# Optimization experiments

Hardware: AMD Instinct MI355X
Metric: run time of the kernel (lower is better)

The kernel has to match this reference:

```python
import jax, jax.numpy as jnp
import numpy as np

N_HEADS, EMB_DIM, K_DIM, V_DIM = 16, 1024, 64, 64
B, L = 4, 2048


def setup_inputs() -> dict:
    key = jax.random.key(0)
    ks = jax.random.split(key, 7)
    scale = 1.0 / np.sqrt(EMB_DIM)
    return {
        "query": jax.random.normal(ks[0], (B, L, EMB_DIM), dtype=jnp.float32),
        "key": jax.random.normal(ks[1], (B, L, EMB_DIM), dtype=jnp.float32),
        "value": jax.random.normal(ks[2], (B, L, EMB_DIM), dtype=jnp.float32),
        "pad_mask": jnp.ones((B, L), dtype=jnp.int32),
        # Linear weights stored as (in, out); torch Linear computes x @ W.T with W (out, in)
        "Wq": jax.random.normal(ks[3], (EMB_DIM, N_HEADS * K_DIM), dtype=jnp.float32) * scale,
        "Wk": jax.random.normal(ks[4], (EMB_DIM, N_HEADS * K_DIM), dtype=jnp.float32) * scale,
        "Wv": jax.random.normal(ks[5], (EMB_DIM, N_HEADS * V_DIM), dtype=jnp.float32) * scale,
        "Wo": jax.random.normal(ks[6], (N_HEADS * V_DIM, EMB_DIM), dtype=jnp.float32) * scale,
    }


def reference(query, key, value, pad_mask, Wq, Wk, Wv, Wo):
    batch, Lq, _ = query.shape
    Lk = key.shape[1]
    # projections -> [B, L, H, dk/dv]
    q = (query @ Wq).reshape(batch, Lq, N_HEADS, K_DIM)
    k = (key @ Wk).reshape(batch, Lk, N_HEADS, K_DIM)
    v = (value @ Wv).reshape(batch, Lk, N_HEADS, V_DIM)
    # logits: [B, H, Lq, Lk], scaled by 1/sqrt(dk)
    logits = jnp.einsum("bqhd,bkhd->bhqk", q, k) / np.sqrt(K_DIM).astype(np.float32)
    # causal mask: disallow j > i
    causal = jnp.tril(jnp.ones((Lq, Lk), dtype=bool))
    logits = jnp.where(causal[None, None], logits, -jnp.inf)
    # pad mask: positions with pad_mask == 0 are masked out
    keep = (pad_mask != 0)[:, None, None, :]  # [B,1,1,Lk]
    logits = jnp.where(keep, logits, -jnp.inf)
    probs = jax.nn.softmax(logits, axis=-1)
    attn = jnp.einsum("bhqk,bkhd->bqhd", probs, v).reshape(batch, Lq, N_HEADS * V_DIM)
    return attn @ Wo
```

## Files before the change

kernel.cpp:

```cpp
#include <hip/hip_runtime.h>
#include <hip/hip_bf16.h>

typedef short bf16x8 __attribute__((ext_vector_type(8)));
typedef float f32x4 __attribute__((ext_vector_type(4)));

#define EMB 1024
#define NH 16
#define SEQ 2048
#define BATCH 4
#define MROWS (BATCH * SEQ)

static __device__ inline unsigned short f2bf(float f) {
  unsigned u = __float_as_uint(f);
  u += 0x7fffu + ((u >> 16) & 1u);
  return (unsigned short)(u >> 16);
}

static __device__ inline unsigned cvtpk(float lo, float hi) {
  unsigned r;
  asm("v_cvt_pk_bf16_f32 %0, %1, %2" : "=v"(r) : "v"(lo), "v"(hi));
  return r;
}

static __device__ inline void gload16(const void* g, void* l) {
  __builtin_amdgcn_global_load_lds(
      (const __attribute__((address_space(1))) unsigned int*)g,
      (__attribute__((address_space(3))) unsigned int*)l, 16, 0, 0);
}

__global__ __launch_bounds__(256) void wtrans_kernel(
    const float* w0, const float* w1, const float* w2, const float* w3,
    unsigned short* o0, unsigned short* o1, unsigned short* o2, unsigned short* o3) {
  __shared__ float t[32][33];
  int z = blockIdx.z;
  const float* W = z == 0 ? w0 : z == 1 ? w1 : z == 2 ? w2 : w3;
  unsigned short* O = z == 0 ? o0 : z == 1 ? o1 : z == 2 ? o2 : o3;
  float sc = (z == 0) ? 0.18033688011112042f : 1.0f;
  int bx = blockIdx.x * 32;
  int by = blockIdx.y * 32;
  int tx = threadIdx.x, ty = threadIdx.y;
#pragma unroll
  for (int j = 0; j < 4; ++j)
    t[ty + j * 8][tx] = W[(size_t)(bx + ty + j * 8) * EMB + by + tx];
  __syncthreads();
#pragma unroll
  for (int j = 0; j < 4; ++j)
    O[(size_t)(by + ty + j * 8) * EMB + bx + tx] = f2bf(t[tx][ty + j * 8] * sc);
}

template <int IN_F32, int OUT_MODE>
__global__ __launch_bounds__(256) void gemm_kernel(const void* Ap, const unsigned short* Bt, void* Cp) {
  __shared__ __align__(16) unsigned short As[128 * 64];
  __shared__ __align__(16) unsigned short Bs[128 * 64];
  const int K = EMB;
  int tid = threadIdx.x;
  int lane = tid & 63, wave = tid >> 6;
  int q = lane & 15, g = lane >> 4;
  int qx7 = q & 7;
  int wm = (wave >> 1) * 64, wn = (wave & 1) * 64;
  int lin = blockIdx.x + (blockIdx.y << 3);
  int idx = (lin & 7) * 64 + (lin >> 3);
  int tm = (idx >> 3) * 128, tn = (idx & 7) * 128;
  f32x4 acc[4][4] = {};
  for (int kt = 0; kt < K; kt += 64) {
    if (IN_F32) {
      const float* A = (const float*)Ap;
#pragma unroll
      for (int it = 0; it < 4; ++it) {
        int gid = tid + it * 256;
        int row = gid >> 3, cb = gid & 7;
        const float4* s0 = (const float4*)(A + (size_t)(tm + row) * K + kt + cb * 8);
        float4 x = s0[0], y = s0[1];
        uint4 w;
        w.x = cvtpk(x.x, x.y); w.y = cvtpk(x.z, x.w);
        w.z = cvtpk(y.x, y.y); w.w = cvtpk(y.z, y.w);
        *(uint4*)&As[row * 64 + 8 * (cb ^ (row & 7))] = w;
      }
    } else {
      const unsigned short* A = (const unsigned short*)Ap;
#pragma unroll
      for (int it = 0; it < 4; ++it) {
        int gid = tid + it * 256;
        int row = gid >> 3, cb = gid & 7;
        gload16(A + (size_t)(tm + row) * K + kt + 8 * (cb ^ (row & 7)), &As[gid * 8]);
      }
    }
#pragma unroll
    for (int it = 0; it < 4; ++it) {
      int gid = tid + it * 256;
      int row = gid >> 3, cb = gid & 7;
      gload16(Bt + (size_t)(tn + row) * K + kt + 8 * (cb ^ (row & 7)), &Bs[gid * 8]);
    }
    __syncthreads();
#pragma unroll
    for (int s = 0; s < 2; ++s) {
      bf16x8 af[4], bfr[4];
#pragma unroll
      for (int mf = 0; mf < 4; ++mf)
        af[mf] = *(const bf16x8*)&As[(wm + mf * 16 + q) * 64 + 8 * ((4 * s + g) ^ qx7)];
#pragma unroll
      for (int nf = 0; nf < 4; ++nf)
        bfr[nf] = *(const bf16x8*)&Bs[(wn + nf * 16 + q) * 64 + 8 * ((4 * s + g) ^ qx7)];
#pragma unroll
      for (int mf = 0; mf < 4; ++mf)
#pragma unroll
        for (int nf = 0; nf < 4; ++nf)
          acc[mf][nf] = __builtin_amdgcn_mfma_f32_16x16x32_bf16(af[mf], bfr[nf], acc[mf][nf], 0, 0, 0);
    }
    __syncthreads();
  }
  if (OUT_MODE == 0) {
    unsigned short* C = (unsigned short*)Cp;
#pragma unroll
    for (int mf = 0; mf < 4; ++mf)
#pragma unroll
      for (int nf = 0; nf < 4; ++nf)
#pragma unroll
        for (int r = 0; r < 4; ++r) {
          int row = tm + wm + mf * 16 + 4 * g + r;
          int col = tn + wn + nf * 16 + q;
          C[(size_t)row * EMB + col] = f2bf(acc[mf][nf][r]);
        }
  } else if (OUT_MODE == 1) {
    unsigned short* C = (unsigned short*)Cp;
#pragma unroll
    for (int mf = 0; mf < 4; ++mf) {
      int m0 = tm + wm + mf * 16 + 4 * g;
      int b = m0 >> 11, l = m0 & 2047;
#pragma unroll
      for (int nf = 0; nf < 4; ++nf) {
        int n = tn + wn + nf * 16 + q;
        int h = n >> 6, dv = n & 63;
        uint2 w;
        w.x = cvtpk(acc[mf][nf][0], acc[mf][nf][1]);
        w.y = cvtpk(acc[mf][nf][2], acc[mf][nf][3]);
        *(uint2*)&C[(((size_t)b * NH + h) * 64 + dv) * SEQ + l] = w;
      }
    }
  } else {
    float* C = (float*)Cp;
#pragma unroll
    for (int mf = 0; mf < 4; ++mf)
#pragma unroll
      for (int nf = 0; nf < 4; ++nf)
#pragma unroll
        for (int r = 0; r < 4; ++r) {
          int row = tm + wm + mf * 16 + 4 * g + r;
          int col = tn + wn + nf * 16 + q;
          C[(size_t)row * EMB + col] = acc[mf][nf][r];
        }
  }
}

__global__ __launch_bounds__(256) void attn_kernel(
    const unsigned short* Qb, const unsigned short* Kb, const unsigned short* VTb,
    const int* pad, unsigned short* Ob) {
  __shared__ __align__(16) unsigned short Ks[2][64 * 64];
  __shared__ __align__(16) unsigned short Vs[2][64 * 64];
  __shared__ __align__(16) unsigned short Ps[4][16 * 64];
  int tid = threadIdx.x;
  int lane = tid & 63, wave = tid >> 6;
  int q = lane & 15, g = lane >> 4;
  int qx7 = q & 7;
  int lin = blockIdx.x;
  int idx = (lin & 7) * 128 + (lin >> 3);
  int b = idx >> 8, h = (idx >> 4) & 15, px = idx & 15;
  int cA = px, cB = 31 - px;

  unsigned allvalid = 0;
#pragma unroll 8
  for (int t0 = 0; t0 < 32; ++t0) {
    int pv = pad[b * SEQ + t0 * 64 + lane];
    if (__ballot(pv != 0) == ~0ull) allvalid |= (1u << t0);
  }

  int qgA = cA * 64 + wave * 16 + q;
  int qgB = cB * 64 + wave * 16 + q;
  const unsigned short* QrowA = Qb + ((size_t)(b * SEQ + qgA)) * EMB + h * 64;
  const unsigned short* QrowB = Qb + ((size_t)(b * SEQ + qgB)) * EMB + h * 64;
  bf16x8 qfA0 = *(const bf16x8*)(QrowA + 8 * g);
  bf16x8 qfA1 = *(const bf16x8*)(QrowA + 32 + 8 * g);
  bf16x8 qfB0 = *(const bf16x8*)(QrowB + 8 * g);
  bf16x8 qfB1 = *(const bf16x8*)(QrowB + 32 + 8 * g);

  bf16x8 ones;
#pragma unroll
  for (int i = 0; i < 8; ++i) ones[i] = (short)0x3F80;

  int srow = tid >> 3, scb = tid & 7;
  int ssw = 8 * (scb ^ (srow & 7));
  const unsigned short* Kbase = Kb + (size_t)b * SEQ * EMB + (size_t)srow * EMB + h * 64 + ssw;
  const unsigned short* Vbase = VTb + (((size_t)(b * NH + h)) * 64 + srow) * SEQ + ssw;

#pragma unroll 1
  for (int half = 0; half < 2; ++half) {
    int c = half ? cB : cA;
    int qg = half ? qgB : qgA;
    bf16x8 qf0 = half ? qfB0 : qfA0;
    bf16x8 qf1 = half ? qfB1 : qfA1;
    f32x4 o[4] = {};
    f32x4 ol = {};
    float m_run = 0.f;

#pragma unroll
    for (int it = 0; it < 2; ++it) {
      gload16(Kbase + (size_t)(it * 32) * EMB, &Ks[0][(tid + it * 256) * 8]);
      gload16(Vbase + (size_t)(it * 32) * SEQ, &Vs[0][(tid + it * 256) * 8]);
    }
    __syncthreads();

#pragma unroll 1
    for (int t = 0; t <= c; ++t) {
      int kvt = t * 64;
      int cur = t & 1;
      if (t < c) {
#pragma unroll
        for (int it = 0; it < 2; ++it) {
          gload16(Kbase + (size_t)(kvt + 64 + it * 32) * EMB, &Ks[cur ^ 1][(tid + it * 256) * 8]);
          gload16(Vbase + (size_t)(kvt + 64) + (size_t)(it * 32) * SEQ, &Vs[cur ^ 1][(tid + it * 256) * 8]);
        }
      }
      bool tilefull = (allvalid >> t) & 1;

      f32x4 sf[4];
      f32x4 seed = {-m_run, -m_run, -m_run, -m_run};
#pragma unroll
      for (int mf = 0; mf < 4; ++mf) sf[mf] = seed;
      __builtin_amdgcn_s_setprio(1);
#pragma unroll
      for (int s = 0; s < 2; ++s) {
#pragma unroll
        for (int mf = 0; mf < 4; ++mf) {
          bf16x8 kf = *(const bf16x8*)&Ks[cur][(mf * 16 + q) * 64 + 8 * ((4 * s + g) ^ qx7)];
          sf[mf] = __builtin_amdgcn_mfma_f32_16x16x32_bf16(kf, s ? qf1 : qf0, sf[mf], 0, 0, 0);
        }
      }
      __builtin_amdgcn_s_setprio(0);

      if (t == c || !tilefull) {
        unsigned long long pmask =
            tilefull ? ~0ull : __ballot(pad[b * SEQ + kvt + lane] != 0);
#pragma unroll
        for (int mf = 0; mf < 4; ++mf)
#pragma unroll
          for (int r = 0; r < 4; ++r) {
            int kvl = mf * 16 + 4 * g + r;
            bool keep = (kvt + kvl <= qg) && ((pmask >> kvl) & 1ULL);
            sf[mf][r] = keep ? sf[mf][r] : -INFINITY;
          }
      }

      float pvv[16];
#pragma unroll
      for (int mf = 0; mf < 4; ++mf)
#pragma unroll
        for (int r = 0; r < 4; ++r)
          pvv[mf * 4 + r] = __builtin_amdgcn_exp2f(sf[mf][r]);

      float t0 = fmaxf(fmaxf(sf[0][0], sf[0][1]), fmaxf(sf[0][2], sf[0][3]));
      float t1 = fmaxf(fmaxf(sf[1][0], sf[1][1]), fmaxf(sf[1][2], sf[1][3]));
      float t2 = fmaxf(fmaxf(sf[2][0], sf[2][1]), fmaxf(sf[2][2], sf[2][3]));
      float t3 = fmaxf(fmaxf(sf[3][0], sf[3][1]), fmaxf(sf[3][2], sf[3][3]));
      float tl = fmaxf(fmaxf(t0, t1), fmaxf(t2, t3));

      if (!__all(tl <= 8.0f)) {
        float tmax = fmaxf(tl, __shfl_xor(tl, 16));
        tmax = fmaxf(tmax, __shfl_xor(tmax, 32));
        float d = fmaxf(tmax, 0.f);
        float alpha = __builtin_amdgcn_exp2f(-d);
        ol[0] *= alpha;
#pragma unroll
        for (int mv = 0; mv < 4; ++mv) o[mv] *= alpha;
#pragma unroll
        for (int mf = 0; mf < 4; ++mf)
#pragma unroll
          for (int r = 0; r < 4; ++r) {
            sf[mf][r] -= d;
            pvv[mf * 4 + r] = __builtin_amdgcn_exp2f(sf[mf][r]);
          }
        m_run += d;
      }

#pragma unroll
      for (int mf = 0; mf < 4; ++mf) {
        uint2 w;
        w.x = cvtpk(pvv[mf * 4 + 0], pvv[mf * 4 + 1]);
        w.y = cvtpk(pvv[mf * 4 + 2], pvv[mf * 4 + 3]);
        int cbP = 2 * mf + (g >> 1);
        *(uint2*)&Ps[wave][q * 64 + 8 * (cbP ^ qx7) + 4 * (g & 1)] = w;
      }

      __builtin_amdgcn_s_setprio(1);
#pragma unroll
      for (int s = 0; s < 2; ++s) {
        bf16x8 pb = *(const bf16x8*)&Ps[wave][q * 64 + 8 * ((4 * s + g) ^ qx7)];
#pragma unroll
        for (int mv = 0; mv < 4; ++mv) {
          bf16x8 va = *(const bf16x8*)&Vs[cur][(mv * 16 + q) * 64 + 8 * ((4 * s + g) ^ qx7)];
          o[mv] = __builtin_amdgcn_mfma_f32_16x16x32_bf16(va, pb, o[mv], 0, 0, 0);
        }
        ol = __builtin_amdgcn_mfma_f32_16x16x32_bf16(ones, pb, ol, 0, 0, 0);
      }
      __builtin_amdgcn_s_setprio(0);
      __syncthreads();
    }

    float inv = 1.0f / ol[0];
    unsigned short* Orow = Ob + ((size_t)(b * SEQ + qg)) * EMB + h * 64;
#pragma unroll
    for (int mv = 0; mv < 4; ++mv) {
      uint2 w;
      w.x = cvtpk(o[mv][0] * inv, o[mv][1] * inv);
      w.y = cvtpk(o[mv][2] * inv, o[mv][3] * inv);
      *(uint2*)&Orow[mv * 16 + 4 * g] = w;
    }
  }
}

extern "C" void kernel_launch(void* const* d_in, const int* in_sizes, int n_in,
                              void* d_out, int out_size, void* d_ws, size_t ws_size,
                              hipStream_t stream) {
  const float* query = (const float*)d_in[0];
  const float* key   = (const float*)d_in[1];
  const float* value = (const float*)d_in[2];
  const int*   pad   = (const int*)d_in[3];
  const float* Wq = (const float*)d_in[4];
  const float* Wk = (const float*)d_in[5];
  const float* Wv = (const float*)d_in[6];
  const float* Wo = (const float*)d_in[7];

  unsigned short* WqT = (unsigned short*)d_ws;
  unsigned short* WkT = WqT + (size_t)EMB * EMB;
  unsigned short* WvT = WkT + (size_t)EMB * EMB;
  unsigned short* WoT = WvT + (size_t)EMB * EMB;
  unsigned short* Qb  = WoT + (size_t)EMB * EMB;
  unsigned short* Kb  = Qb + (size_t)MROWS * EMB;
  unsigned short* VTb = Kb + (size_t)MROWS * EMB;
  unsigned short* Ab  = VTb + (size_t)MROWS * EMB;

  wtrans_kernel<<<dim3(EMB / 32, EMB / 32, 4), dim3(32, 8), 0, stream>>>(
      Wq, Wk, Wv, Wo, WqT, WkT, WvT, WoT);
  gemm_kernel<1, 0><<<dim3(8, 64), 256, 0, stream>>>(query, WqT, Qb);
  gemm_kernel<1, 0><<<dim3(8, 64), 256, 0, stream>>>(key, WkT, Kb);
  gemm_kernel<1, 1><<<dim3(8, 64), 256, 0, stream>>>(value, WvT, VTb);
  attn_kernel<<<dim3(1024), 256, 0, stream>>>(Qb, Kb, VTb, pad, Ab);
  gemm_kernel<0, 2><<<dim3(8, 64), 256, 0, stream>>>(Ab, WoT, (float*)d_out);
}
```

Baseline: 202.3 us.

## Double query rows per wave in attention to reuse K/V tiles across 128-row blocks

The attention kernel now gives each wave two 16-row query fragments (32 rows), so each block covers 128 query rows and the grid is halved to 512 blocks. Each K/V tile loaded into shared memory feeds twice as many MFMAs, which cuts global and LDS traffic per unit of work. Waves whose rows lie entirely before a tile skip its compute. The costs are more registers per wave, a larger P buffer in shared memory, fewer blocks for occupancy, and some idle waves on the causal-diagonal tiles.

```diff
diff --git a/kernel.cpp b/kernel.cpp
--- a/kernel.cpp
+++ b/kernel.cpp
@@ -157,15 +157,14 @@
     const int* pad, unsigned short* Ob) {
   __shared__ __align__(16) unsigned short Ks[2][64 * 64];
   __shared__ __align__(16) unsigned short Vs[2][64 * 64];
-  __shared__ __align__(16) unsigned short Ps[4][16 * 64];
+  __shared__ __align__(16) unsigned short Ps[4][32 * 64];
   int tid = threadIdx.x;
   int lane = tid & 63, wave = tid >> 6;
   int q = lane & 15, g = lane >> 4;
   int qx7 = q & 7;
   int lin = blockIdx.x;
-  int idx = (lin & 7) * 128 + (lin >> 3);
-  int b = idx >> 8, h = (idx >> 4) & 15, px = idx & 15;
-  int cA = px, cB = 31 - px;
+  int idx = (lin & 7) * 64 + (lin >> 3);
+  int b = idx >> 7, h = (idx >> 3) & 15, px = idx & 7;
 
   unsigned allvalid = 0;
 #pragma unroll 8
@@ -174,15 +173,6 @@
     if (__ballot(pv != 0) == ~0ull) allvalid |= (1u << t0);
   }
 
-  int qgA = cA * 64 + wave * 16 + q;
-  int qgB = cB * 64 + wave * 16 + q;
-  const unsigned short* QrowA = Qb + ((size_t)(b * SEQ + qgA)) * EMB + h * 64;
-  const unsigned short* QrowB = Qb + ((size_t)(b * SEQ + qgB)) * EMB + h * 64;
-  bf16x8 qfA0 = *(const bf16x8*)(QrowA + 8 * g);
-  bf16x8 qfA1 = *(const bf16x8*)(QrowA + 32 + 8 * g);
-  bf16x8 qfB0 = *(const bf16x8*)(QrowB + 8 * g);
-  bf16x8 qfB1 = *(const bf16x8*)(QrowB + 32 + 8 * g);
-
   bf16x8 ones;
 #pragma unroll
   for (int i = 0; i < 8; ++i) ones[i] = (short)0x3F80;
@@ -194,13 +184,21 @@
 
 #pragma unroll 1
   for (int half = 0; half < 2; ++half) {
-    int c = half ? cB : cA;
-    int qg = half ? qgB : qgA;
-    bf16x8 qf0 = half ? qfB0 : qfA0;
-    bf16x8 qf1 = half ? qfB1 : qfA1;
-    f32x4 o[4] = {};
-    f32x4 ol = {};
-    float m_run = 0.f;
+    int c = half ? 15 - px : px;
+    int tend = 2 * c + 1;
+    int qbase = c * 128 + wave * 32;
+    int qgA = qbase + q;
+    int qgB = qbase + 16 + q;
+    const unsigned short* QrowA = Qb + ((size_t)(b * SEQ + qgA)) * EMB + h * 64;
+    const unsigned short* QrowB = Qb + ((size_t)(b * SEQ + qgB)) * EMB + h * 64;
+    bf16x8 qA0 = *(const bf16x8*)(QrowA + 8 * g);
+    bf16x8 qA1 = *(const bf16x8*)(QrowA + 32 + 8 * g);
+    bf16x8 qB0 = *(const bf16x8*)(QrowB + 8 * g);
+    bf16x8 qB1 = *(const bf16x8*)(QrowB + 32 + 8 * g);
+
+    f32x4 oA[4] = {}, oB[4] = {};
+    f32x4 olA = {}, olB = {};
+    float mA = 0.f, mB = 0.f;
 
 #pragma unroll
     for (int it = 0; it < 2; ++it) {
@@ -210,109 +208,161 @@
     __syncthreads();
 
 #pragma unroll 1
-    for (int t = 0; t <= c; ++t) {
+    for (int t = 0; t <= tend; ++t) {
       int kvt = t * 64;
       int cur = t & 1;
-      if (t < c) {
+      if (t < tend) {
 #pragma unroll
         for (int it = 0; it < 2; ++it) {
           gload16(Kbase + (size_t)(kvt + 64 + it * 32) * EMB, &Ks[cur ^ 1][(tid + it * 256) * 8]);
           gload16(Vbase + (size_t)(kvt + 64) + (size_t)(it * 32) * SEQ, &Vs[cur ^ 1][(tid + it * 256) * 8]);
         }
       }
-      bool tilefull = (allvalid >> t) & 1;
-
-      f32x4 sf[4];
-      f32x4 seed = {-m_run, -m_run, -m_run, -m_run};
-#pragma unroll
-      for (int mf = 0; mf < 4; ++mf) sf[mf] = seed;
-      __builtin_amdgcn_s_setprio(1);
-#pragma unroll
-      for (int s = 0; s < 2; ++s) {
-#pragma unroll
-        for (int mf = 0; mf < 4; ++mf) {
-          bf16x8 kf = *(const bf16x8*)&Ks[cur][(mf * 16 + q) * 64 + 8 * ((4 * s + g) ^ qx7)];
-          sf[mf] = __builtin_amdgcn_mfma_f32_16x16x32_bf16(kf, s ? qf1 : qf0, sf[mf], 0, 0, 0);
-        }
-      }
-      __builtin_amdgcn_s_setprio(0);
-
-      if (t == c || !tilefull) {
-        unsigned long long pmask =
-            tilefull ? ~0ull : __ballot(pad[b * SEQ + kvt + lane] != 0);
-#pragma unroll
-        for (int mf = 0; mf < 4; ++mf)
-#pragma unroll
-          for (int r = 0; r < 4; ++r) {
-            int kvl = mf * 16 + 4 * g + r;
-            bool keep = (kvt + kvl <= qg) && ((pmask >> kvl) & 1ULL);
-            sf[mf][r] = keep ? sf[mf][r] : -INFINITY;
-          }
-      }
-
-      float pvv[16];
-#pragma unroll
-      for (int mf = 0; mf < 4; ++mf)
-#pragma unroll
-        for (int r = 0; r < 4; ++r)
-          pvv[mf * 4 + r] = __builtin_amdgcn_exp2f(sf[mf][r]);
-
-      float t0 = fmaxf(fmaxf(sf[0][0], sf[0][1]), fmaxf(sf[0][2], sf[0][3]));
-      float t1 = fmaxf(fmaxf(sf[1][0], sf[1][1]), fmaxf(sf[1][2], sf[1][3]));
-      float t2 = fmaxf(fmaxf(sf[2][0], sf[2][1]), fmaxf(sf[2][2], sf[2][3]));
-      float t3 = fmaxf(fmaxf(sf[3][0], sf[3][1]), fmaxf(sf[3][2], sf[3][3]));
-      float tl = fmaxf(fmaxf(t0, t1), fmaxf(t2, t3));
-
-      if (!__all(tl <= 8.0f)) {
-        float tmax = fmaxf(tl, __shfl_xor(tl, 16));
-        tmax = fmaxf(tmax, __shfl_xor(tmax, 32));
-        float d = fmaxf(tmax, 0.f);
-        float alpha = __builtin_amdgcn_exp2f(-d);
-        ol[0] *= alpha;
-#pragma unroll
-        for (int mv = 0; mv < 4; ++mv) o[mv] *= alpha;
-#pragma unroll
-        for (int mf = 0; mf < 4; ++mf)
-#pragma unroll
-          for (int r = 0; r < 4; ++r) {
-            sf[mf][r] -= d;
-            pvv[mf * 4 + r] = __builtin_amdgcn_exp2f(sf[mf][r]);
-          }
-        m_run += d;
-      }
-
-#pragma unroll
-      for (int mf = 0; mf < 4; ++mf) {
-        uint2 w;
-        w.x = cvtpk(pvv[mf * 4 + 0], pvv[mf * 4 + 1]);
-        w.y = cvtpk(pvv[mf * 4 + 2], pvv[mf * 4 + 3]);
-        int cbP = 2 * mf + (g >> 1);
-        *(uint2*)&Ps[wave][q * 64 + 8 * (cbP ^ qx7) + 4 * (g & 1)] = w;
-      }
-
-      __builtin_amdgcn_s_setprio(1);
-#pragma unroll
-      for (int s = 0; s < 2; ++s) {
-        bf16x8 pb = *(const bf16x8*)&Ps[wave][q * 64 + 8 * ((4 * s + g) ^ qx7)];
-#pragma unroll
-        for (int mv = 0; mv < 4; ++mv) {
-          bf16x8 va = *(const bf16x8*)&Vs[cur][(mv * 16 + q) * 64 + 8 * ((4 * s + g) ^ qx7)];
-          o[mv] = __builtin_amdgcn_mfma_f32_16x16x32_bf16(va, pb, o[mv], 0, 0, 0);
-        }
-        ol = __builtin_amdgcn_mfma_f32_16x16x32_bf16(ones, pb, ol, 0, 0, 0);
-      }
-      __builtin_amdgcn_s_setprio(0);
+      bool active = (kvt < qbase + 32);
+      if (active) {
+        bool tilefull = (allvalid >> t) & 1;
+
+        f32x4 sA[4], sB[4];
+        f32x4 seedA = {-mA, -mA, -mA, -mA};
+        f32x4 seedB = {-mB, -mB, -mB, -mB};
+#pragma unroll
+        for (int mf = 0; mf < 4; ++mf) { sA[mf] = seedA; sB[mf] = seedB; }
+        __builtin_amdgcn_s_setprio(1);
+#pragma unroll
+        for (int s = 0; s < 2; ++s) {
+#pragma unroll
+          for (int mf = 0; mf < 4; ++mf) {
+            bf16x8 kf = *(const bf16x8*)&Ks[cur][(mf * 16 + q) * 64 + 8 * ((4 * s + g) ^ qx7)];
+            sA[mf] = __builtin_amdgcn_mfma_f32_16x16x32_bf16(kf, s ? qA1 : qA0, sA[mf], 0, 0, 0);
+            sB[mf] = __builtin_amdgcn_mfma_f32_16x16x32_bf16(kf, s ? qB1 : qB0, sB[mf], 0, 0, 0);
+          }
+        }
+        __builtin_amdgcn_s_setprio(0);
+
+        if ((kvt + 63 > qbase) || !tilefull) {
+          unsigned long long pmask =
+              tilefull ? ~0ull : __ballot(pad[b * SEQ + kvt + lane] != 0);
+#pragma unroll
+          for (int mf = 0; mf < 4; ++mf)
+#pragma unroll
+            for (int r = 0; r < 4; ++r) {
+              int kvl = mf * 16 + 4 * g + r;
+              int kvg = kvt + kvl;
+              bool bit = (pmask >> kvl) & 1ULL;
+              sA[mf][r] = (kvg <= qgA && bit) ? sA[mf][r] : -INFINITY;
+              sB[mf][r] = (kvg <= qgB && bit) ? sB[mf][r] : -INFINITY;
+            }
+        }
+
+        {
+          float pvv[16];
+#pragma unroll
+          for (int mf = 0; mf < 4; ++mf)
+#pragma unroll
+            for (int r = 0; r < 4; ++r)
+              pvv[mf * 4 + r] = __builtin_amdgcn_exp2f(sA[mf][r]);
+          float t0 = fmaxf(fmaxf(sA[0][0], sA[0][1]), fmaxf(sA[0][2], sA[0][3]));
+          float t1 = fmaxf(fmaxf(sA[1][0], sA[1][1]), fmaxf(sA[1][2], sA[1][3]));
+          float t2 = fmaxf(fmaxf(sA[2][0], sA[2][1]), fmaxf(sA[2][2], sA[2][3]));
+          float t3 = fmaxf(fmaxf(sA[3][0], sA[3][1]), fmaxf(sA[3][2], sA[3][3]));
+          float tl = fmaxf(fmaxf(t0, t1), fmaxf(t2, t3));
+          if (!__all(tl <= 8.0f)) {
+            float tmax = fmaxf(tl, __shfl_xor(tl, 16));
+            tmax = fmaxf(tmax, __shfl_xor(tmax, 32));
+            float d = fmaxf(tmax, 0.f);
+            float alpha = __builtin_amdgcn_exp2f(-d);
+            olA *= alpha;
+#pragma unroll
+            for (int mv = 0; mv < 4; ++mv) oA[mv] *= alpha;
+#pragma unroll
+            for (int mf = 0; mf < 4; ++mf)
+#pragma unroll
+              for (int r = 0; r < 4; ++r) {
+                sA[mf][r] -= d;
+                pvv[mf * 4 + r] = __builtin_amdgcn_exp2f(sA[mf][r]);
+              }
+            mA += d;
+          }
+#pragma unroll
+          for (int mf = 0; mf < 4; ++mf) {
+            uint2 w;
+            w.x = cvtpk(pvv[mf * 4 + 0], pvv[mf * 4 + 1]);
+            w.y = cvtpk(pvv[mf * 4 + 2], pvv[mf * 4 + 3]);
+            int cbP = 2 * mf + (g >> 1);
+            *(uint2*)&Ps[wave][q * 64 + 8 * (cbP ^ qx7) + 4 * (g & 1)] = w;
+          }
+        }
+        {
+          float pvv[16];
+#pragma unroll
+          for (int mf = 0; mf < 4; ++mf)
+#pragma unroll
+            for (int r = 0; r < 4; ++r)
+              pvv[mf * 4 + r] = __builtin_amdgcn_exp2f(sB[mf][r]);
+          float t0 = fmaxf(fmaxf(sB[0][0], sB[0][1]), fmaxf(sB[0][2], sB[0][3]));
+          float t1 = fmaxf(fmaxf(sB[1][0], sB[1][1]), fmaxf(sB[1][2], sB[1][3]));
+          float t2 = fmaxf(fmaxf(sB[2][0], sB[2][1]), fmaxf(sB[2][2], sB[2][3]));
+          float t3 = fmaxf(fmaxf(sB[3][0], sB[3][1]), fmaxf(sB[3][2], sB[3][3]));
+          float tl = fmaxf(fmaxf(t0, t1), fmaxf(t2, t3));
+          if (!__all(tl <= 8.0f)) {
+            float tmax = fmaxf(tl, __shfl_xor(tl, 16));
+            tmax = fmaxf(tmax, __shfl_xor(tmax, 32));
+            float d = fmaxf(tmax, 0.f);
+            float alpha = __builtin_amdgcn_exp2f(-d);
+            olB *= alpha;
+#pragma unroll
+            for (int mv = 0; mv < 4; ++mv) oB[mv] *= alpha;
+#pragma unroll
+            for (int mf = 0; mf < 4; ++mf)
+#pragma unroll
+              for (int r = 0; r < 4; ++r) {
+                sB[mf][r] -= d;
+                pvv[mf * 4 + r] = __builtin_amdgcn_exp2f(sB[mf][r]);
+              }
+            mB += d;
+          }
+#pragma unroll
+          for (int mf = 0; mf < 4; ++mf) {
+            uint2 w;
+            w.x = cvtpk(pvv[mf * 4 + 0], pvv[mf * 4 + 1]);
+            w.y = cvtpk(pvv[mf * 4 + 2], pvv[mf * 4 + 3]);
+            int cbP = 2 * mf + (g >> 1);
+            *(uint2*)&Ps[wave][(16 + q) * 64 + 8 * (cbP ^ qx7) + 4 * (g & 1)] = w;
+          }
+        }
+
+        __builtin_amdgcn_s_setprio(1);
+#pragma unroll
+        for (int s = 0; s < 2; ++s) {
+          bf16x8 pbA = *(const bf16x8*)&Ps[wave][q * 64 + 8 * ((4 * s + g) ^ qx7)];
+          bf16x8 pbB = *(const bf16x8*)&Ps[wave][(16 + q) * 64 + 8 * ((4 * s + g) ^ qx7)];
+#pragma unroll
+          for (int mv = 0; mv < 4; ++mv) {
+            bf16x8 va = *(const bf16x8*)&Vs[cur][(mv * 16 + q) * 64 + 8 * ((4 * s + g) ^ qx7)];
+            oA[mv] = __builtin_amdgcn_mfma_f32_16x16x32_bf16(va, pbA, oA[mv], 0, 0, 0);
+            oB[mv] = __builtin_amdgcn_mfma_f32_16x16x32_bf16(va, pbB, oB[mv], 0, 0, 0);
+          }
+          olA = __builtin_amdgcn_mfma_f32_16x16x32_bf16(ones, pbA, olA, 0, 0, 0);
+          olB = __builtin_amdgcn_mfma_f32_16x16x32_bf16(ones, pbB, olB, 0, 0, 0);
+        }
+        __builtin_amdgcn_s_setprio(0);
+      }
       __syncthreads();
     }
 
-    float inv = 1.0f / ol[0];
-    unsigned short* Orow = Ob + ((size_t)(b * SEQ + qg)) * EMB + h * 64;
+    float invA = 1.0f / olA[0];
+    float invB = 1.0f / olB[0];
+    unsigned short* OrowA = Ob + ((size_t)(b * SEQ + qgA)) * EMB + h * 64;
+    unsigned short* OrowB = Ob + ((size_t)(b * SEQ + qgB)) * EMB + h * 64;
 #pragma unroll
     for (int mv = 0; mv < 4; ++mv) {
-      uint2 w;
-      w.x = cvtpk(o[mv][0] * inv, o[mv][1] * inv);
-      w.y = cvtpk(o[mv][2] * inv, o[mv][3] * inv);
-      *(uint2*)&Orow[mv * 16 + 4 * g] = w;
+      uint2 wa, wb;
+      wa.x = cvtpk(oA[mv][0] * invA, oA[mv][1] * invA);
+      wa.y = cvtpk(oA[mv][2] * invA, oA[mv][3] * invA);
+      wb.x = cvtpk(oB[mv][0] * invB, oB[mv][1] * invB);
+      wb.y = cvtpk(oB[mv][2] * invB, oB[mv][3] * invB);
+      *(uint2*)&OrowA[mv * 16 + 4 * g] = wa;
+      *(uint2*)&OrowB[mv * 16 + 4 * g] = wb;
     }
   }
 }
@@ -343,6 +393,6 @@
   gemm_kernel<1, 0><<<dim3(8, 64), 256, 0, stream>>>(query, WqT, Qb);
   gemm_kernel<1, 0><<<dim3(8, 64), 256, 0, stream>>>(key, WkT, Kb);
   gemm_kernel<1, 1><<<dim3(8, 64), 256, 0, stream>>>(value, WvT, VTb);
-  attn_kernel<<<dim3(1024), 256, 0, stream>>>(Qb, Kb, VTb, pad, Ab);
+  attn_kernel<<<dim3(512), 256, 0, stream>>>(Qb, Kb, VTb, pad, Ab);
   gemm_kernel<0, 2><<<dim3(8, 64), 256, 0, stream>>>(Ab, WoT, (float*)d_out);
 }
```

Measured after the change: 189.4 us. 1.07x faster.
